# Optimization experiments

Hardware: AMD Instinct MI355X
Metric: run time of the kernel (lower is better)

Reference implementation:

```python
import jax, jax.numpy as jnp
import numpy as np

N_NODES = 100000
N_EDGES = 6400000
IN_CH, HID, OUT_CH = 128, 16, 32


def setup_inputs() -> dict:
    key = jax.random.key(0)
    k1, k2, k3, k4 = jax.random.split(key, 4)
    x = jax.random.normal(k1, (N_NODES, IN_CH), dtype=jnp.float32)
    edge_index = jax.random.randint(k2, (2, N_EDGES), 0, N_NODES, dtype=jnp.int64)
    # glorot-ish scaled weights
    W1 = jax.random.normal(k3, (IN_CH, HID), dtype=jnp.float32) * (1.0 / np.sqrt(IN_CH))
    W2 = jax.random.normal(k4, (HID, OUT_CH), dtype=jnp.float32) * (1.0 / np.sqrt(HID))
    b1 = jnp.zeros((HID,), dtype=jnp.float32)
    b2 = jnp.zeros((OUT_CH,), dtype=jnp.float32)
    return {"x": x, "edge_index": edge_index, "W1": W1, "b1": b1, "W2": W2, "b2": b2}


def reference(x, edge_index, W1, b1, W2, b2):
    N = x.shape[0]
    # PyG GCNConv: add self-loops, symmetric D^{-1/2} A D^{-1/2} normalization
    loop = jnp.arange(N, dtype=edge_index.dtype)
    src = jnp.concatenate([edge_index[0], loop])  # [E+N]
    dst = jnp.concatenate([edge_index[1], loop])  # [E+N]
    deg = jax.ops.segment_sum(jnp.ones_like(dst, dtype=x.dtype), dst, num_segments=N)
    deg_inv_sqrt = jnp.where(deg > 0, jax.lax.rsqrt(deg), 0.0)
    norm = deg_inv_sqrt[src] * deg_inv_sqrt[dst]  # [E+N]

    def gcn_conv(h, W, b):
        h = h @ W                                   # transform first (small out dim)
        msg = h[src] * norm[:, None]                # gather + scale
        agg = jax.ops.segment_sum(msg, dst, num_segments=N)  # scatter-add
        return agg + b

    h = jax.nn.relu(gcn_conv(x, W1, b1))
    return gcn_conv(h, W2, b2)
```

## Files before the change

### kernel.cpp

```cpp
#include <hip/hip_runtime.h>


#define IN_CH 128
#define HID 16
#define OUT_CH 32

#define TILE 8192
#define BSHIFT 8
#define BNODES 256
#define BCAP 17408
#define NBUCK_MAX 512

typedef __attribute__((ext_vector_type(4))) _Float16 half4;

__global__ __launch_bounds__(512) void bucket_kernel(
    const int* __restrict__ src, const int* __restrict__ dst,
    int* __restrict__ bcur, int* __restrict__ bpacked, int E, int nbuck) {
  __shared__ int stage[TILE];
  __shared__ unsigned char stg_b[TILE];
  __shared__ int hist[NBUCK_MAX];
  __shared__ int scn[NBUCK_MAX];
  __shared__ int cur[NBUCK_MAX];
  __shared__ int gbase[NBUCK_MAX];

  int tid = threadIdx.x;
  int base = blockIdx.x * TILE;
  int cnt_t = E - base; if (cnt_t > TILE) cnt_t = TILE;
  bool full = (cnt_t == TILE);

  hist[tid] = 0;
  __syncthreads();

  int4 d4[4], s4[4];
  if (full) {
    const int4* dv = (const int4*)(dst + base);
    #pragma unroll
    for (int k = 0; k < 4; ++k) d4[k] = dv[tid + 512 * k];
    #pragma unroll
    for (int k = 0; k < 4; ++k) {
      atomicAdd(&hist[d4[k].x >> BSHIFT], 1);
      atomicAdd(&hist[d4[k].y >> BSHIFT], 1);
      atomicAdd(&hist[d4[k].z >> BSHIFT], 1);
      atomicAdd(&hist[d4[k].w >> BSHIFT], 1);
    }
    const int4* sv = (const int4*)(src + base);
    #pragma unroll
    for (int k = 0; k < 4; ++k) s4[k] = sv[tid + 512 * k];
  } else {
    for (int i = tid; i < cnt_t; i += 512)
      atomicAdd(&hist[dst[base + i] >> BSHIFT], 1);
  }
  __syncthreads();
  scn[tid] = hist[tid];
  __syncthreads();
  for (int off = 1; off < 512; off <<= 1) {
    int a0 = (tid >= off) ? scn[tid - off] : 0;
    __syncthreads();
    scn[tid] += a0;
    __syncthreads();
  }
  {
    int b = tid;
    int excl = scn[b] - hist[b];
    cur[b] = excl;
    int c = hist[b];
    gbase[b] = (b < nbuck && c > 0) ? atomicAdd(&bcur[b], c) : 0;
  }
  __syncthreads();
  if (full) {
    #pragma unroll
    for (int k = 0; k < 4; ++k) {
      int dd[4] = {d4[k].x, d4[k].y, d4[k].z, d4[k].w};
      int ss[4] = {s4[k].x, s4[k].y, s4[k].z, s4[k].w};
      #pragma unroll
      for (int c = 0; c < 4; ++c) {
        int d = dd[c], s = ss[c];
        int b = d >> BSHIFT;
        int r = atomicAdd(&cur[b], 1);
        stage[r] = ((b >> 8) << 25) | ((d & 255) << 17) | s;
        stg_b[r] = (unsigned char)b;
      }
    }
  } else {
    for (int i = tid; i < cnt_t; i += 512) {
      int d = dst[base + i];
      int s = src[base + i];
      int b = d >> BSHIFT;
      int r = atomicAdd(&cur[b], 1);
      stage[r] = ((b >> 8) << 25) | ((d & 255) << 17) | s;
      stg_b[r] = (unsigned char)b;
    }
  }
  __syncthreads();
  for (int i = tid; i < cnt_t; i += 512) {
    int sv = stage[i];
    int b = stg_b[i] | (((sv >> 25) & 1) << 8);
    int excl = scn[b] - hist[b];
    int pos = gbase[b] + (i - excl);
    if (pos < BCAP) bpacked[(size_t)b * BCAP + pos] = sv & 0x1FFFFFF;
  }
}

__global__ __launch_bounds__(1024) void nodesort_kernel(
    const int* __restrict__ bpacked, const int* __restrict__ bcur,
    int* __restrict__ csr, int* __restrict__ row_ptr, int* __restrict__ cnt,
    float* __restrict__ dis, int N) {
  __shared__ int h[BNODES];
  __shared__ int sc[BNODES];
  __shared__ int cu[BNODES];
  int b = blockIdx.x;
  int tid = threadIdx.x;
  if (tid < BNODES) h[tid] = 0;
  __syncthreads();
  int ecnt = bcur[b]; if (ecnt > BCAP) ecnt = BCAP;
  int ecnt4 = ecnt & ~3;
  const int* bp = bpacked + (size_t)b * BCAP;
  const int4* bp4 = (const int4*)bp;

  int4 p[5];
  bool g[5];
  #pragma unroll
  for (int k = 0; k < 5; ++k) {
    int i4 = tid + k * 1024;
    g[k] = (i4 * 4 < ecnt4);
    if (g[k]) p[k] = bp4[i4];
  }
  int tl = 0;
  bool gt = (ecnt4 + tid < ecnt);
  if (gt) tl = bp[ecnt4 + tid];

  #pragma unroll
  for (int k = 0; k < 5; ++k) {
    if (g[k]) {
      atomicAdd(&h[(p[k].x >> 17) & 255], 1);
      atomicAdd(&h[(p[k].y >> 17) & 255], 1);
      atomicAdd(&h[(p[k].z >> 17) & 255], 1);
      atomicAdd(&h[(p[k].w >> 17) & 255], 1);
    }
  }
  if (gt) atomicAdd(&h[(tl >> 17) & 255], 1);
  __syncthreads();
  if (tid < BNODES) sc[tid] = h[tid];
  __syncthreads();
  for (int off = 1; off < BNODES; off <<= 1) {
    int t = 0;
    if (tid < BNODES && tid >= off) t = sc[tid - off];
    __syncthreads();
    if (tid < BNODES) sc[tid] += t;
    __syncthreads();
  }
  if (tid < BNODES) cu[tid] = sc[tid] - h[tid];
  __syncthreads();
  int* cb = csr + (size_t)b * BCAP;
  #pragma unroll
  for (int k = 0; k < 5; ++k) {
    if (g[k]) {
      int r;
      r = atomicAdd(&cu[(p[k].x >> 17) & 255], 1); cb[r] = p[k].x & 0x1FFFF;
      r = atomicAdd(&cu[(p[k].y >> 17) & 255], 1); cb[r] = p[k].y & 0x1FFFF;
      r = atomicAdd(&cu[(p[k].z >> 17) & 255], 1); cb[r] = p[k].z & 0x1FFFF;
      r = atomicAdd(&cu[(p[k].w >> 17) & 255], 1); cb[r] = p[k].w & 0x1FFFF;
    }
  }
  if (gt) {
    int r = atomicAdd(&cu[(tl >> 17) & 255], 1);
    cb[r] = tl & 0x1FFFF;
  }
  if (tid < BNODES) {
    int node = (b << BSHIFT) + tid;
    if (node < N) {
      row_ptr[node] = b * BCAP + (sc[tid] - h[tid]);
      cnt[node] = h[tid];
      dis[node] = rsqrtf((float)h[tid] + 1.0f);
    }
  }
}

__global__ __launch_bounds__(256) void gemm1_kernel(
    const float* __restrict__ x, const float* __restrict__ W1,
    const float* __restrict__ dis, _Float16* __restrict__ t1h, int N) {
  __shared__ __align__(16) float xs[64 * 132];
  __shared__ __align__(16) float w1s[128 * 16];
  int tid = threadIdx.x;
  int nb = blockIdx.x * 64;
  for (int i = tid; i < 128 * 16; i += 256) w1s[i] = W1[i];
  int maxRows = N - nb; if (maxRows > 64) maxRows = 64;
  const float4* xg = (const float4*)(x + (size_t)nb * IN_CH);
  for (int i = tid; i < maxRows * 32; i += 256) {
    float4 v = xg[i];
    int row = i >> 5;
    int k4 = (i & 31) << 2;
    *((float4*)&xs[row * 132 + k4]) = v;
  }
  __syncthreads();
  int nl = tid >> 2;
  int cg = tid & 3;
  int node = nb + nl;
  float4 acc = make_float4(0.f, 0.f, 0.f, 0.f);
  const float* xrow = &xs[nl * 132];
  const float4* w4 = (const float4*)w1s;
  for (int k = 0; k < 128; ++k) {
    float xv = xrow[k];
    float4 wv = w4[k * 4 + cg];
    acc.x += xv * wv.x; acc.y += xv * wv.y;
    acc.z += xv * wv.z; acc.w += xv * wv.w;
  }
  if (node < N) {
    float dd = dis[node];
    half4 hv;
    hv.x = (_Float16)(acc.x * dd);
    hv.y = (_Float16)(acc.y * dd);
    hv.z = (_Float16)(acc.z * dd);
    hv.w = (_Float16)(acc.w * dd);
    *((half4*)&t1h[(size_t)node * HID + cg * 4]) = hv;
  }
}

template <bool RELU>
__global__ __launch_bounds__(256) void ggather_kernel(
    const int* __restrict__ row_ptr, const int* __restrict__ cnt,
    const int* __restrict__ csr, const float* __restrict__ dis,
    const _Float16* __restrict__ feat, const float* __restrict__ bias,
    const float* __restrict__ W2, const float* __restrict__ b2,
    _Float16* __restrict__ out16, float* __restrict__ outp, int N) {
  __shared__ __align__(16) float w2s[16 * 32];
  __shared__ __align__(16) float b2s[32];
  int tid = threadIdx.x;
  if (!RELU) {
    for (int i = tid; i < 16 * 32; i += 256) w2s[i] = W2[i];
    if (tid < 32) b2s[tid] = b2[tid];
    __syncthreads();
  }
  int gid = blockIdx.x * 256 + tid;
  int node = gid >> 4;
  if (node >= N) return;
  int sub = gid & 15;
  int par = sub >> 2;
  int q4 = (sub & 3) << 2;
  int beg = row_ptr[node];
  int c = cnt[node];
  const int* row = csr + beg;
  half4 sf = *(const half4*)(feat + (size_t)node * HID + q4);
  float dd = dis[node];
  float ax = 0.f, ay = 0.f, az = 0.f, aw = 0.f;
  int j = par;
  for (; j + 28 < c; j += 32) {
    int s[8];
    #pragma unroll
    for (int e = 0; e < 8; ++e) s[e] = row[j + 4 * e];
    half4 f[8];
    #pragma unroll
    for (int e = 0; e < 8; ++e)
      f[e] = *(const half4*)(feat + (size_t)s[e] * HID + q4);
    #pragma unroll
    for (int e = 0; e < 8; ++e) {
      ax += (float)f[e].x; ay += (float)f[e].y;
      az += (float)f[e].z; aw += (float)f[e].w;
    }
  }
  for (; j < c; j += 4) {
    int s = row[j];
    half4 f = *(const half4*)(feat + (size_t)s * HID + q4);
    ax += (float)f.x; ay += (float)f.y; az += (float)f.z; aw += (float)f.w;
  }
  ax += __shfl_down(ax, 4); ax += __shfl_down(ax, 8);
  ay += __shfl_down(ay, 4); ay += __shfl_down(ay, 8);
  az += __shfl_down(az, 4); az += __shfl_down(az, 8);
  aw += __shfl_down(aw, 4); aw += __shfl_down(aw, 8);
  if (RELU) {
    if (sub < 4) {
      float rx = dd * (ax + (float)sf.x);
      float ry = dd * (ay + (float)sf.y);
      float rz = dd * (az + (float)sf.z);
      float rw = dd * (aw + (float)sf.w);
      float4 bb = *(const float4*)(bias + q4);
      rx = fmaxf(rx + bb.x, 0.f) * dd;
      ry = fmaxf(ry + bb.y, 0.f) * dd;
      rz = fmaxf(rz + bb.z, 0.f) * dd;
      rw = fmaxf(rw + bb.w, 0.f) * dd;
      half4 hv;
      hv.x = (_Float16)rx; hv.y = (_Float16)ry;
      hv.z = (_Float16)rz; hv.w = (_Float16)rw;
      *((half4*)&out16[(size_t)node * HID + q4]) = hv;
    }
  } else {
    float rv0 = dd * (ax + (float)sf.x);
    float rv1 = dd * (ay + (float)sf.y);
    float rv2 = dd * (az + (float)sf.z);
    float rv3 = dd * (aw + (float)sf.w);
    int lane = tid & 63;
    int base16 = lane & ~15;
    int k = lane & 15;
    float a0 = b2s[2 * k], a1 = b2s[2 * k + 1];
    #pragma unroll
    for (int q = 0; q < 4; ++q) {
      float c0 = __shfl(rv0, base16 + q);
      float c1 = __shfl(rv1, base16 + q);
      float c2 = __shfl(rv2, base16 + q);
      float c3 = __shfl(rv3, base16 + q);
      const float* w0 = &w2s[(4 * q + 0) * 32 + 2 * k];
      const float* w1 = &w2s[(4 * q + 1) * 32 + 2 * k];
      const float* w2p = &w2s[(4 * q + 2) * 32 + 2 * k];
      const float* w3 = &w2s[(4 * q + 3) * 32 + 2 * k];
      a0 += c0 * w0[0] + c1 * w1[0] + c2 * w2p[0] + c3 * w3[0];
      a1 += c0 * w0[1] + c1 * w1[1] + c2 * w2p[1] + c3 * w3[1];
    }
    float2 r2; r2.x = a0; r2.y = a1;
    *((float2*)&outp[(size_t)node * OUT_CH + 2 * k]) = r2;
  }
}

extern "C" void kernel_launch(void* const* d_in, const int* in_sizes, int n_in,
                              void* d_out, int out_size, void* d_ws, size_t ws_size,
                              hipStream_t stream) {
  const float* x  = (const float*)d_in[0];
  const int* ei   = (const int*)d_in[1];
  const float* W1 = (const float*)d_in[2];
  const float* b1 = (const float*)d_in[3];
  const float* W2 = (const float*)d_in[4];
  const float* b2 = (const float*)d_in[5];
  float* out = (float*)d_out;

  int N = in_sizes[0] / IN_CH;
  int E = in_sizes[1] / 2;
  const int* src = ei;
  const int* dst = ei + E;

  int nbuck = (N + BNODES - 1) >> BSHIFT;

  int*      bcur    = (int*)d_ws;
  float*    dis     = (float*)(bcur + 512);
  int*      row_ptr = (int*)(dis + N);
  int*      cnt     = row_ptr + N;
  _Float16* t1h     = (_Float16*)(cnt + N);
  _Float16* h1h     = t1h + (size_t)N * HID;
  int*      bpacked = (int*)(h1h + (size_t)N * HID);
  int*      csr     = bpacked + (size_t)nbuck * BCAP;

  hipMemsetAsync(bcur, 0, 512 * sizeof(int), stream);

  bucket_kernel<<<(E + TILE - 1) / TILE, 512, 0, stream>>>(
      src, dst, bcur, bpacked, E, nbuck);
  nodesort_kernel<<<nbuck, 1024, 0, stream>>>(
      bpacked, bcur, csr, row_ptr, cnt, dis, N);
  gemm1_kernel<<<(N + 63) / 64, 256, 0, stream>>>(x, W1, dis, t1h, N);
  ggather_kernel<true><<<((size_t)N * 16 + 255) / 256, 256, 0, stream>>>(
      row_ptr, cnt, csr, dis, t1h, b1, nullptr, nullptr, h1h, nullptr, N);
  ggather_kernel<false><<<((size_t)N * 16 + 255) / 256, 256, 0, stream>>>(
      row_ptr, cnt, csr, dis, h1h, nullptr, W2, b2, nullptr, out, N);
}
```

Before: 284.2 us.

## Fuse first-layer GEMM into the node-sort kernel

Merges the separate x@W1 GEMM kernel into the per-bucket node-sort kernel, so each 256-node bucket block also computes its rows of t1h in two 128-row chunks, using the in-LDS degree histogram to apply the normalization directly. This removes one kernel launch and the dependency on reading dis from global memory. In exchange the nodesort block uses roughly 76 KB more LDS, which can lower occupancy. The GEMM also runs on only ~391 blocks instead of ~1563, with 2 outputs per thread instead of 4.

```diff
diff --git a/kernel.cpp b/kernel.cpp
--- a/kernel.cpp
+++ b/kernel.cpp
@@ -12,6 +12,7 @@
 #define NBUCK_MAX 512
 
 typedef __attribute__((ext_vector_type(4))) _Float16 half4;
+typedef __attribute__((ext_vector_type(2))) _Float16 half2v;
 
 __global__ __launch_bounds__(512) void bucket_kernel(
     const int* __restrict__ src, const int* __restrict__ dst,
@@ -101,16 +102,21 @@
   }
 }
 
-__global__ __launch_bounds__(1024) void nodesort_kernel(
+__global__ __launch_bounds__(1024) void nodesort_gemm_kernel(
     const int* __restrict__ bpacked, const int* __restrict__ bcur,
+    const float* __restrict__ x, const float* __restrict__ W1,
     int* __restrict__ csr, int* __restrict__ row_ptr, int* __restrict__ cnt,
-    float* __restrict__ dis, int N) {
+    float* __restrict__ dis, _Float16* __restrict__ t1h, int N) {
   __shared__ int h[BNODES];
   __shared__ int sc[BNODES];
   __shared__ int cu[BNODES];
+  __shared__ __align__(16) float w1s[128 * 16];
+  __shared__ __align__(16) float xs[128 * 132];
   int b = blockIdx.x;
   int tid = threadIdx.x;
   if (tid < BNODES) h[tid] = 0;
+  #pragma unroll
+  for (int k = 0; k < 2; ++k) w1s[tid + 1024 * k] = W1[tid + 1024 * k];
   __syncthreads();
   int ecnt = bcur[b]; if (ecnt > BCAP) ecnt = BCAP;
   int ecnt4 = ecnt & ~3;
@@ -174,45 +180,37 @@
       dis[node] = rsqrtf((float)h[tid] + 1.0f);
     }
   }
-}
-
-__global__ __launch_bounds__(256) void gemm1_kernel(
-    const float* __restrict__ x, const float* __restrict__ W1,
-    const float* __restrict__ dis, _Float16* __restrict__ t1h, int N) {
-  __shared__ __align__(16) float xs[64 * 132];
-  __shared__ __align__(16) float w1s[128 * 16];
-  int tid = threadIdx.x;
-  int nb = blockIdx.x * 64;
-  for (int i = tid; i < 128 * 16; i += 256) w1s[i] = W1[i];
-  int maxRows = N - nb; if (maxRows > 64) maxRows = 64;
-  const float4* xg = (const float4*)(x + (size_t)nb * IN_CH);
-  for (int i = tid; i < maxRows * 32; i += 256) {
-    float4 v = xg[i];
-    int row = i >> 5;
-    int k4 = (i & 31) << 2;
-    *((float4*)&xs[row * 132 + k4]) = v;
-  }
-  __syncthreads();
-  int nl = tid >> 2;
-  int cg = tid & 3;
-  int node = nb + nl;
-  float4 acc = make_float4(0.f, 0.f, 0.f, 0.f);
-  const float* xrow = &xs[nl * 132];
-  const float4* w4 = (const float4*)w1s;
-  for (int k = 0; k < 128; ++k) {
-    float xv = xrow[k];
-    float4 wv = w4[k * 4 + cg];
-    acc.x += xv * wv.x; acc.y += xv * wv.y;
-    acc.z += xv * wv.z; acc.w += xv * wv.w;
-  }
-  if (node < N) {
-    float dd = dis[node];
-    half4 hv;
-    hv.x = (_Float16)(acc.x * dd);
-    hv.y = (_Float16)(acc.y * dd);
-    hv.z = (_Float16)(acc.z * dd);
-    hv.w = (_Float16)(acc.w * dd);
-    *((half4*)&t1h[(size_t)node * HID + cg * 4]) = hv;
+
+  int nl = tid >> 3;
+  int ch2 = (tid & 7) << 1;
+  #pragma unroll
+  for (int chunk = 0; chunk < 2; ++chunk) {
+    int nbase = (b << BSHIFT) + (chunk << 7);
+    __syncthreads();
+    const float4* xg = (const float4*)(x + (size_t)nbase * IN_CH);
+    for (int i = tid; i < 128 * 32; i += 1024) {
+      int row = i >> 5;
+      int k4 = (i & 31) << 2;
+      float4 v = make_float4(0.f, 0.f, 0.f, 0.f);
+      if (nbase + row < N) v = xg[i];
+      *((float4*)&xs[row * 132 + k4]) = v;
+    }
+    __syncthreads();
+    int node = nbase + nl;
+    float a0 = 0.f, a1 = 0.f;
+    const float* xrow = &xs[nl * 132];
+    for (int k = 0; k < 128; ++k) {
+      float xv = xrow[k];
+      a0 += xv * w1s[k * 16 + ch2];
+      a1 += xv * w1s[k * 16 + ch2 + 1];
+    }
+    if (node < N) {
+      float dd = rsqrtf((float)h[(chunk << 7) + nl] + 1.0f);
+      half2v hv;
+      hv.x = (_Float16)(a0 * dd);
+      hv.y = (_Float16)(a1 * dd);
+      *((half2v*)&t1h[(size_t)node * HID + ch2]) = hv;
+    }
   }
 }
 
@@ -341,9 +339,8 @@
 
   bucket_kernel<<<(E + TILE - 1) / TILE, 512, 0, stream>>>(
       src, dst, bcur, bpacked, E, nbuck);
-  nodesort_kernel<<<nbuck, 1024, 0, stream>>>(
-      bpacked, bcur, csr, row_ptr, cnt, dis, N);
-  gemm1_kernel<<<(N + 63) / 64, 256, 0, stream>>>(x, W1, dis, t1h, N);
+  nodesort_gemm_kernel<<<nbuck, 1024, 0, stream>>>(
+      bpacked, bcur, x, W1, csr, row_ptr, cnt, dis, t1h, N);
   ggather_kernel<true><<<((size_t)N * 16 + 255) / 256, 256, 0, stream>>>(
       row_ptr, cnt, csr, dis, t1h, b1, nullptr, nullptr, h1h, nullptr, N);
   ggather_kernel<false><<<((size_t)N * 16 + 255) / 256, 256, 0, stream>>>(
```

Result: no change. 280.6 us (-1.3%).
